# Kernel optimization log

Measured on AMD Instinct MI355X. Metric: run time of the kernel, lower is better.

Reference implementation:

```python
import jax, jax.numpy as jnp
import numpy as np

N_NODES = 50000
N_EDGES = 800000
F = 53
B = 128
H = 4


def _p(key, shape, scale=0.1):
    return jax.random.normal(key, shape, dtype=jnp.float32) * scale


def setup_inputs() -> dict:
    key = jax.random.key(0)
    ks = jax.random.split(key, 40)
    inp = {
        'x': jax.random.normal(ks[0], (N_NODES, F), dtype=jnp.float32),
        'edge_index': jax.random.randint(ks[1], (2, N_EDGES), 0, N_NODES),
        'batch': jnp.sort(jax.random.randint(ks[2], (N_NODES,), 0, B)),
        # GATConv(53 -> 53, heads=4)
        'gat_w': _p(ks[3], (F, H * F)),
        'gat_att_src': _p(ks[4], (H, F)),
        'gat_att_dst': _p(ks[5], (H, F)),
        'gat_bias': _p(ks[6], (H * F,)),
        # GINConv MLP: 53 -> 106 -> 106
        'gin_w1': _p(ks[7], (F, 2 * F)), 'gin_b1': _p(ks[8], (2 * F,)),
        'gin_w2': _p(ks[9], (2 * F, 2 * F)), 'gin_b2': _p(ks[10], (2 * F,)),
        # EdgeConv MLP: 106 -> 106 -> 106
        'ec_w1': _p(ks[11], (2 * F, 2 * F)), 'ec_b1': _p(ks[12], (2 * F,)),
        'ec_w2': _p(ks[13], (2 * F, 2 * F)), 'ec_b2': _p(ks[14], (2 * F,)),
        # per-branch heads
        'fg1_w': _p(ks[15], (4 * F, 256)), 'fg1_b': _p(ks[16], (256,)),
        'fg2_w': _p(ks[17], (256, 128)), 'fg2_b': _p(ks[18], (128,)),
        'fg3_w': _p(ks[19], (2 * F, 256)), 'fg3_b': _p(ks[20], (256,)),
        'fg4_w': _p(ks[21], (256, 128)), 'fg4_b': _p(ks[22], (128,)),
        'fg5_w': _p(ks[23], (2 * F, 256)), 'fg5_b': _p(ks[24], (256,)),
        'fg6_w': _p(ks[25], (256, 128)), 'fg6_b': _p(ks[26], (128,)),
        # final MLP
        'fc1_w': _p(ks[27], (384, 128)), 'fc1_b': _p(ks[28], (128,)),
        'fc2_w': _p(ks[29], (128, 64)), 'fc2_b': _p(ks[30], (64,)),
        'out_w': _p(ks[31], (64, 1)), 'out_b': _p(ks[32], (1,)),
    }
    return inp


def _gat(x, src, dst, w, a_src, a_dst, bias):
    # PyG GATConv with add_self_loops=True, negative_slope=0.2, concat heads
    n = x.shape[0]
    loop = jnp.arange(n)
    s = jnp.concatenate([src, loop])
    d = jnp.concatenate([dst, loop])
    xh = (x @ w).reshape(n, H, F)                      # [N,H,F]
    al_s = jnp.einsum('nhf,hf->nh', xh, a_src)         # [N,H]
    al_d = jnp.einsum('nhf,hf->nh', xh, a_dst)
    e = jax.nn.leaky_relu(al_s[s] + al_d[d], 0.2)      # [E2,H]
    m = jax.ops.segment_max(e, d, num_segments=n)
    ex = jnp.exp(e - m[d])
    z = jax.ops.segment_sum(ex, d, num_segments=n)
    alpha = ex / (z[d] + 1e-16)                        # softmax over in-edges
    msg = xh[s] * alpha[:, :, None]                    # [E2,H,F]
    out = jax.ops.segment_sum(msg, d, num_segments=n)
    return out.reshape(n, H * F) + bias


def _gin(x, src, dst, w1, b1, w2, b2):
    # PyG GINConv, eps=0: nn(x + sum_j x_j)
    n = x.shape[0]
    agg = jax.ops.segment_sum(x[src], dst, num_segments=n)
    h = x + agg
    return jax.nn.relu(h @ w1 + b1) @ w2 + b2


def _edgeconv(x, src, dst, w1, b1, w2, b2):
    # PyG EdgeConv: max_j nn([x_i, x_j - x_i]) at target i
    n = x.shape[0]
    xi = x[dst]
    feat = jnp.concatenate([xi, x[src] - xi], axis=-1)  # [E,2F]
    h = jax.nn.relu(feat @ w1 + b1) @ w2 + b2
    out = jax.ops.segment_max(h, dst, num_segments=n)
    return jnp.where(jnp.isfinite(out), out, 0.0)       # empty segments -> 0


def _gep(x, batch):
    # global mean pool per graph
    s = jax.ops.segment_sum(x, batch, num_segments=B)
    cnt = jax.ops.segment_sum(jnp.ones((x.shape[0],), x.dtype), batch, num_segments=B)
    return s / jnp.maximum(cnt, 1.0)[:, None]


def reference(x, edge_index, batch,
              gat_w, gat_att_src, gat_att_dst, gat_bias,
              gin_w1, gin_b1, gin_w2, gin_b2,
              ec_w1, ec_b1, ec_w2, ec_b2,
              fg1_w, fg1_b, fg2_w, fg2_b, fg3_w, fg3_b,
              fg4_w, fg4_b, fg5_w, fg5_b, fg6_w, fg6_b,
              fc1_w, fc1_b, fc2_w, fc2_b, out_w, out_b):
    relu = jax.nn.relu
    src, dst = edge_index[0], edge_index[1]

    xt = relu(_gat(x, src, dst, gat_w, gat_att_src, gat_att_dst, gat_bias))
    xt = _gep(xt, batch)
    xt = relu(xt @ fg1_w + fg1_b)
    xt = relu(xt @ fg2_w + fg2_b)

    xt2 = relu(_gin(x, src, dst, gin_w1, gin_b1, gin_w2, gin_b2))
    xt2 = _gep(xt2, batch)
    xt2 = relu(xt2 @ fg3_w + fg3_b)
    xt2 = relu(xt2 @ fg4_w + fg4_b)

    xt3 = relu(_edgeconv(x, src, dst, ec_w1, ec_b1, ec_w2, ec_b2))
    xt3 = _gep(xt3, batch)
    xt3 = relu(xt3 @ fg5_w + fg5_b)
    xt3 = relu(xt3 @ fg6_w + fg6_b)

    h = jnp.concatenate([xt, xt2, xt3], axis=1)         # [B,384]
    h = relu(h @ fc1_w + fc1_b)
    h = relu(h @ fc2_w + fc2_b)
    return jax.nn.sigmoid(h @ out_w + out_b)            # [B,1]
```

## Files before the change

kernel.cpp:

```cpp
#include <hip/hip_runtime.h>
#include <hip/hip_bf16.h>
#include <math.h>

#define N_NODES 50000
#define N_EDGES 800000
#define FDIM 53
#define BATCH 128
#define HF 212
#define F2 106
#define POOLW 424
#define NPK2 220
#define PSTR 32
#define ECS 128
#define A4P 256

typedef __attribute__((ext_vector_type(8))) short short8;
typedef __attribute__((ext_vector_type(4))) float f32x4;

__device__ __forceinline__ float leaky02(float x){ return x >= 0.f ? x : 0.2f * x; }

__device__ __forceinline__ short f2bf(float x) {
  unsigned u = __float_as_uint(x);
  unsigned r = (u + 0x7fffu + ((u >> 16) & 1u)) >> 16;
  return (short)r;
}
__device__ __forceinline__ float bf2f(short b) {
  return __uint_as_float(((unsigned)(unsigned short)b) << 16);
}
__device__ __forceinline__ unsigned pk2(float a, float b) {
  union { __hip_bfloat162 h; unsigned u; } c;
  c.h = __float22bfloat162_rn(make_float2(a, b));
  return c.u;
}
__device__ __forceinline__ void ldsbar() {
  __builtin_amdgcn_s_waitcnt(0xC07F);
  __builtin_amdgcn_s_barrier();
}

__global__ void k_prep(const float* __restrict__ ec_w1, const float* __restrict__ ec_b1,
                       const float* __restrict__ gat_w, const float* __restrict__ asrc,
                       const float* __restrict__ adst,
                       float* __restrict__ Wp, float* __restrict__ bp) {
  int idx = blockIdx.x * blockDim.x + threadIdx.x;
  if (idx < FDIM * NPK2) {
    int k = idx / NPK2, j = idx % NPK2;
    float v;
    if (j < F2)            v = ec_w1[k * F2 + j] - ec_w1[(FDIM + k) * F2 + j];
    else if (j < 2 * F2)   v = ec_w1[(FDIM + k) * F2 + (j - F2)];
    else {
      int r = j - 2 * F2;
      int sd = r >> 2, h = r & 3;
      const float* av = sd ? adst : asrc;
      float acc = 0.f;
      for (int f = 0; f < FDIM; ++f)
        acc += gat_w[k * HF + h * FDIM + f] * av[h * FDIM + f];
      v = acc;
    }
    Wp[idx] = v;
  }
  if (idx < NPK2) {
    bp[idx] = (idx < F2) ? ec_b1[idx] : 0.f;
  }
}

#define GM 64
#define GN 110
#define GNP 112
#define APAD 57
__global__ __launch_bounds__(256) void k_gemm(
    const float* __restrict__ x, const float* __restrict__ Wp, const float* __restrict__ bp,
    short* __restrict__ xb, short* __restrict__ Ub, short* __restrict__ Vb,
    float* __restrict__ alS, float* __restrict__ alD) {
  __shared__ float As[GM * APAD];
  __shared__ float Ws[FDIM * GNP];
  int mb = blockIdx.x >> 1, nc = blockIdx.x & 1;
  int m0 = mb * GM, n0 = nc * GN;
  int t = threadIdx.x;
  for (int idx = t; idx < GM * FDIM; idx += 256) {
    int m = idx / FDIM, k = idx % FDIM;
    int gm = m0 + m;
    float v = (gm < N_NODES) ? x[(size_t)gm * FDIM + k] : 0.f;
    As[m * APAD + k] = v;
    if (nc == 0 && gm < N_NODES) xb[(size_t)gm * 64 + k] = f2bf(v);
  }
  for (int idx = t; idx < FDIM * GNP; idx += 256) {
    int k = idx / GNP, n = idx % GNP;
    Ws[idx] = (n < GN) ? Wp[k * NPK2 + n0 + n] : 0.f;
  }
  __syncthreads();
  int tx = t & 15, ty = t >> 4;
  int ms = tx * 4, ns = ty * 7;
  float acc[4][7];
#pragma unroll
  for (int i = 0; i < 4; i++)
#pragma unroll
    for (int j = 0; j < 7; j++) acc[i][j] = 0.f;
  for (int k = 0; k < FDIM; k++) {
    float a0 = As[(ms + 0) * APAD + k];
    float a1 = As[(ms + 1) * APAD + k];
    float a2 = As[(ms + 2) * APAD + k];
    float a3 = As[(ms + 3) * APAD + k];
    float b[7];
#pragma unroll
    for (int j = 0; j < 7; j++) b[j] = Ws[k * GNP + ns + j];
#pragma unroll
    for (int j = 0; j < 7; j++) {
      acc[0][j] += a0 * b[j];
      acc[1][j] += a1 * b[j];
      acc[2][j] += a2 * b[j];
      acc[3][j] += a3 * b[j];
    }
  }
  float bj[7];
#pragma unroll
  for (int j = 0; j < 7; j++) {
    int g = n0 + ns + j;
    bj[j] = (g < NPK2) ? bp[g] : 0.f;
  }
#pragma unroll
  for (int i = 0; i < 4; i++) {
    int gm = m0 + ms + i;
    if (gm >= N_NODES) break;
#pragma unroll
    for (int j = 0; j < 7; j++) {
      int g = n0 + ns + j;
      float v = acc[i][j] + bj[j];
      if (g < F2)             Ub[(size_t)gm * ECS + g] = f2bf(v);
      else if (g < 2 * F2)    Vb[(size_t)gm * ECS + (g - F2)] = f2bf(v);
      else if (g < 2 * F2 + 4) alS[gm * 4 + (g - 2 * F2)] = v;
      else if (g < NPK2)      alD[gm * 4 + (g - 2 * F2 - 4)] = v;
    }
  }
}

#define SCAN_BLOCKS ((N_NODES + 255) / 256)

__global__ void k_hist(const int* __restrict__ ei, int* __restrict__ histP) {
  int t = blockIdx.x * blockDim.x + threadIdx.x;
  if (t < N_EDGES) atomicAdd(&histP[ei[N_EDGES + t] << 5], 1);
}

__global__ __launch_bounds__(256) void k_scan1(const int* __restrict__ histP,
                                               const int* __restrict__ batch,
                                               int* __restrict__ rp, int* __restrict__ bsum,
                                               int* __restrict__ start) {
  __shared__ int buf[256];
  int tid = threadIdx.x;
  int idx = blockIdx.x * 256 + tid;
  int v = (idx < N_NODES) ? histP[idx << 5] : 0;
  buf[tid] = v;
  __syncthreads();
  for (int off = 1; off < 256; off <<= 1) {
    int t2 = (tid >= off) ? buf[tid - off] : 0;
    __syncthreads();
    buf[tid] += t2;
    __syncthreads();
  }
  if (idx < N_NODES) rp[idx] = buf[tid] - v;
  if (tid == 255) bsum[blockIdx.x] = buf[255];
  if (idx < N_NODES) {
    int b = batch[idx];
    if (idx == 0)
      for (int g = 0; g <= b; g++) start[g] = 0;
    int bn = (idx + 1 < N_NODES) ? batch[idx + 1] : BATCH;
    for (int g = b + 1; g <= bn; g++) start[g] = idx + 1;
  }
}

__global__ __launch_bounds__(256) void k_scan3(const int* __restrict__ bsum,
                                               int* __restrict__ rp, int* __restrict__ histP) {
  __shared__ int buf[256];
  int tid = threadIdx.x;
  int v = (tid < SCAN_BLOCKS) ? bsum[tid] : 0;
  buf[tid] = v;
  __syncthreads();
  for (int off = 1; off < 256; off <<= 1) {
    int t2 = (tid >= off) ? buf[tid - off] : 0;
    __syncthreads();
    buf[tid] += t2;
    __syncthreads();
  }
  int boff = (blockIdx.x == 0) ? 0 : buf[blockIdx.x - 1];
  int idx = blockIdx.x * 256 + tid;
  if (idx < N_NODES) {
    int o = rp[idx] + boff;
    rp[idx] = o;
    histP[idx << 5] = o;
  }
  if (idx == 0) rp[N_NODES] = N_EDGES;
}

__global__ void k_scatter(const int* __restrict__ ei, int* __restrict__ histP,
                          int* __restrict__ colidx) {
  int e = blockIdx.x * blockDim.x + threadIdx.x;
  if (e >= N_EDGES) return;
  int d = ei[N_EDGES + e];
  int pos = atomicAdd(&histP[d << 5], 1);
  colidx[pos] = ei[e];
}

#define GCH 20
__global__ __launch_bounds__(256) void k_gatgin(
    const short* __restrict__ xb, const float* __restrict__ alS, const float* __restrict__ alD,
    const int* __restrict__ rp, const int* __restrict__ colidx,
    short* __restrict__ agg4, float* __restrict__ agg) {
  int wid = threadIdx.x >> 6, lane = threadIdx.x & 63;
  bool fa = lane < FDIM;
  int i0 = blockIdx.x * GCH;
  int iend = min(i0 + GCH, N_NODES);
  __shared__ int rpG[GCH + 1];
  __shared__ int sL[4][64];
  __shared__ float4 eL[4][64];
  {
    int t = threadIdx.x, nn = iend - i0;
    if (t <= nn) rpG[t] = rp[i0 + t];
  }
  __syncthreads();
  for (int i = i0 + wid; i < iend; i += 4) {
    int base = rpG[i - i0], deg = rpG[i - i0 + 1] - base;
    float4 adv = *(const float4*)(alD + (size_t)i * 4);
    float4 asv = *(const float4*)(alS + (size_t)i * 4);
    float aldi[4] = {adv.x, adv.y, adv.z, adv.w};
    float exs[4];
    exs[0] = __expf(leaky02(asv.x + aldi[0]));
    exs[1] = __expf(leaky02(asv.y + aldi[1]));
    exs[2] = __expf(leaky02(asv.z + aldi[2]));
    exs[3] = __expf(leaky02(asv.w + aldi[3]));
    float xiv = fa ? bf2f(xb[(size_t)i * 64 + lane]) : 0.f;
    float ag0 = exs[0] * xiv, ag1 = exs[1] * xiv, ag2 = exs[2] * xiv, ag3 = exs[3] * xiv;
    float ax = xiv;
    float zl[4] = {0.f, 0.f, 0.f, 0.f};

    for (int c0 = 0; c0 < deg; c0 += 64) {
      int cn = min(64, deg - c0);
      int s = 0;
      float ex0 = 0.f, ex1 = 0.f, ex2 = 0.f, ex3 = 0.f;
      if (lane < cn) {
        s = colidx[base + c0 + lane];
        float4 av = *(const float4*)(alS + (size_t)s * 4);
        ex0 = __expf(leaky02(av.x + aldi[0]));
        ex1 = __expf(leaky02(av.y + aldi[1]));
        ex2 = __expf(leaky02(av.z + aldi[2]));
        ex3 = __expf(leaky02(av.w + aldi[3]));
        zl[0] += ex0; zl[1] += ex1; zl[2] += ex2; zl[3] += ex3;
      }
      sL[wid][lane] = s;
      eL[wid][lane] = make_float4(ex0, ex1, ex2, ex3);
      for (int jj = 0; jj < cn; jj += 4) {
        int4 s4 = *(const int4*)&sL[wid][jj];
        int sj[4] = {s4.x, s4.y, s4.z, s4.w};
        float4 e0 = eL[wid][jj + 0];
        float4 e1 = eL[wid][jj + 1];
        float4 e2 = eL[wid][jj + 2];
        float4 e3 = eL[wid][jj + 3];
        float xg[4];
#pragma unroll
        for (int q = 0; q < 4; q++)
          xg[q] = fa ? bf2f(xb[(size_t)sj[q] * 64 + lane]) : 0.f;
        ag0 += e0.x * xg[0] + e1.x * xg[1] + e2.x * xg[2] + e3.x * xg[3];
        ag1 += e0.y * xg[0] + e1.y * xg[1] + e2.y * xg[2] + e3.y * xg[3];
        ag2 += e0.z * xg[0] + e1.z * xg[1] + e2.z * xg[2] + e3.z * xg[3];
        ag3 += e0.w * xg[0] + e1.w * xg[1] + e2.w * xg[2] + e3.w * xg[3];
#pragma unroll
        for (int q = 0; q < 4; q++)
          if (jj + q < cn) ax += xg[q];
      }
    }
#pragma unroll
    for (int off = 32; off >= 1; off >>= 1)
#pragma unroll
      for (int h = 0; h < 4; h++) zl[h] += __shfl_xor(zl[h], off);
    {
      float z0 = zl[0] + exs[0] + 1e-16f;
      float z1 = zl[1] + exs[1] + 1e-16f;
      float z2 = zl[2] + exs[2] + 1e-16f;
      float z3 = zl[3] + exs[3] + 1e-16f;
      short* ar = agg4 + (size_t)i * A4P;
      ar[0 * 64 + lane] = fa ? f2bf(ag0 / z0) : (short)0;
      ar[1 * 64 + lane] = fa ? f2bf(ag1 / z1) : (short)0;
      ar[2 * 64 + lane] = fa ? f2bf(ag2 / z2) : (short)0;
      ar[3 * 64 + lane] = fa ? f2bf(ag3 / z3) : (short)0;
      if (fa) agg[(size_t)i * FDIM + lane] = ax;
    }
  }
}

#define BTS 72
__global__ __launch_bounds__(256) void k_gt(
    const short* __restrict__ agg4, const float* __restrict__ gat_w,
    const float* __restrict__ gat_b, const int* __restrict__ batch,
    float* __restrict__ pooled) {
  __shared__ short Bt[4 * 56 * BTS];
  __shared__ float psum[4 * 224];
  __shared__ int batL[64];
  int m0 = blockIdx.x * 64;
  int t = threadIdx.x;
  for (int idx = t; idx < 4 * 224; idx += 256) psum[idx] = 0.f;
  if (t < 64) batL[t] = batch[min(m0 + t, N_NODES - 1)];
  for (int idx = t; idx < 4 * 64 * 56; idx += 256) {
    int n = idx % 56, kk = (idx / 56) & 63, h = idx / (56 * 64);
    short v = (kk < FDIM && n < FDIM) ? f2bf(gat_w[kk * HF + h * FDIM + n]) : (short)0;
    Bt[(h * 56 + n) * BTS + kk] = v;
  }
  __syncthreads();
  const int lane = t & 63, wid = t >> 6;
  const int n16 = lane & 15, quad = lane >> 4;
  const int mrow0 = wid * 16;
  const int bmin = batL[0];
  const bool uni = (batL[0] == batL[63]);
  const size_t abase = (size_t)(m0 + mrow0 + n16) * A4P;
#pragma unroll
  for (int h = 0; h < 4; h++) {
    short8 af0 = *(const short8*)(agg4 + abase + h * 64 + quad * 8);
    short8 af1 = *(const short8*)(agg4 + abase + h * 64 + 32 + quad * 8);
#pragma unroll
    for (int nt = 0; nt < 4; nt++) {
      short8 b0 = *(const short8*)&Bt[(h * 56 + nt * 16 + n16) * BTS + quad * 8];
      short8 b1 = *(const short8*)&Bt[(h * 56 + nt * 16 + n16) * BTS + 32 + quad * 8];
      f32x4 acc = {0.f, 0.f, 0.f, 0.f};
      acc = __builtin_amdgcn_mfma_f32_16x16x32_bf16(af0, b0, acc, 0, 0, 0);
      acc = __builtin_amdgcn_mfma_f32_16x16x32_bf16(af1, b1, acc, 0, 0, 0);
      int jn = nt * 16 + n16;
      bool jv = jn < FDIM;
      float bj = jv ? gat_b[h * FDIM + jn] : 0.f;
      if (uni) {
        float s = 0.f;
#pragma unroll
        for (int r = 0; r < 4; r++) {
          int gm = m0 + mrow0 + quad * 4 + r;
          if (gm < N_NODES) s += fmaxf(acc[r] + bj, 0.f);
        }
        s += __shfl_xor(s, 16);
        s += __shfl_xor(s, 32);
        if (quad == 0 && jv && s != 0.f) atomicAdd(&psum[h * 56 + jn], s);
      } else {
        float pj = 0.f; int curb = -1;
#pragma unroll
        for (int r = 0; r < 4; r++) {
          int lm = mrow0 + quad * 4 + r;
          int gm = m0 + lm;
          if (gm < N_NODES) {
            float o = fmaxf(acc[r] + bj, 0.f);
            int b = batL[lm];
            if (b != curb) {
              if (curb >= 0 && jv) {
                int slot = curb - bmin;
                if (slot >= 0 && slot < 4) atomicAdd(&psum[slot * 224 + h * 56 + jn], pj);
                else atomicAdd(&pooled[(size_t)curb * POOLW + h * FDIM + jn], pj);
              }
              curb = b; pj = o;
            } else {
              pj += o;
            }
          }
        }
        if (curb >= 0 && jv) {
          int slot = curb - bmin;
          if (slot >= 0 && slot < 4) atomicAdd(&psum[slot * 224 + h * 56 + jn], pj);
          else atomicAdd(&pooled[(size_t)curb * POOLW + h * FDIM + jn], pj);
        }
      }
    }
  }
  __syncthreads();
  for (int idx = t; idx < 4 * 224; idx += 256) {
    int slot = idx / 224, c = idx % 224;
    int h = c / 56, jn = c % 56;
    float v = psum[idx];
    int b = bmin + slot;
    if (jn < FDIM && b < BATCH && v != 0.f)
      atomicAdd(&pooled[(size_t)b * POOLW + h * FDIM + jn], v);
  }
}

#define A2PAD 111
__global__ __launch_bounds__(256) void k_gin(
    const float* __restrict__ agg,
    const float* __restrict__ w1, const float* __restrict__ b1,
    const float* __restrict__ w2, const float* __restrict__ b2,
    const int* __restrict__ batch, float* __restrict__ pooled) {
  __shared__ float B1[F2 * 112];
  __shared__ float Hs[64 * A2PAD];
  __shared__ float psum[4 * 112];
  float* As = B1;
  float* Ws1 = B1 + 64 * APAD;
  int m0 = blockIdx.x * 64;
  int t = threadIdx.x;
  for (int idx = t; idx < 4 * 112; idx += 256) psum[idx] = 0.f;
  for (int idx = t; idx < 64 * FDIM; idx += 256) {
    int m = idx / FDIM, k = idx % FDIM;
    int gm = m0 + m;
    As[m * APAD + k] = (gm < N_NODES) ? agg[(size_t)gm * FDIM + k] : 0.f;
  }
  for (int idx = t; idx < FDIM * 112; idx += 256) {
    int k = idx / 112, n = idx % 112;
    Ws1[idx] = (n < F2) ? w1[k * F2 + n] : 0.f;
  }
  __syncthreads();
  int tx = t & 15, ty = t >> 4;
  int ms = tx * 4, ns = ty * 7;
  {
    float acc[4][7];
#pragma unroll
    for (int i = 0; i < 4; i++)
#pragma unroll
      for (int j = 0; j < 7; j++) acc[i][j] = 0.f;
    for (int k = 0; k < FDIM; k++) {
      float a0 = As[(ms + 0) * APAD + k];
      float a1 = As[(ms + 1) * APAD + k];
      float a2 = As[(ms + 2) * APAD + k];
      float a3 = As[(ms + 3) * APAD + k];
      float b[7];
#pragma unroll
      for (int j = 0; j < 7; j++) b[j] = Ws1[k * 112 + ns + j];
#pragma unroll
      for (int j = 0; j < 7; j++) {
        acc[0][j] += a0 * b[j];
        acc[1][j] += a1 * b[j];
        acc[2][j] += a2 * b[j];
        acc[3][j] += a3 * b[j];
      }
    }
#pragma unroll
    for (int i = 0; i < 4; i++) {
#pragma unroll
      for (int j = 0; j < 7; j++) {
        int n = ns + j;
        if (n < F2) Hs[(ms + i) * A2PAD + n] = fmaxf(acc[i][j] + b1[n], 0.f);
      }
    }
  }
  __syncthreads();
  for (int idx = t; idx < F2 * 112; idx += 256) {
    int k = idx / 112, n = idx % 112;
    B1[idx] = (n < F2) ? w2[k * F2 + n] : 0.f;
  }
  __syncthreads();
  float acc[4][7];
#pragma unroll
  for (int i = 0; i < 4; i++)
#pragma unroll
    for (int j = 0; j < 7; j++) acc[i][j] = 0.f;
  for (int k = 0; k < F2; k++) {
    float a0 = Hs[(ms + 0) * A2PAD + k];
    float a1 = Hs[(ms + 1) * A2PAD + k];
    float a2 = Hs[(ms + 2) * A2PAD + k];
    float a3 = Hs[(ms + 3) * A2PAD + k];
    float b[7];
#pragma unroll
    for (int j = 0; j < 7; j++) b[j] = B1[k * 112 + ns + j];
#pragma unroll
    for (int j = 0; j < 7; j++) {
      acc[0][j] += a0 * b[j];
      acc[1][j] += a1 * b[j];
      acc[2][j] += a2 * b[j];
      acc[3][j] += a3 * b[j];
    }
  }
  float b2n[7];
#pragma unroll
  for (int j = 0; j < 7; j++) {
    int n = ns + j;
    b2n[j] = (n < F2) ? b2[n] : 0.f;
  }
  int bmin = batch[m0];
  float pj[7];
#pragma unroll
  for (int j = 0; j < 7; j++) pj[j] = 0.f;
  int curb = -1;
#pragma unroll
  for (int i = 0; i < 4; i++) {
    int gm = m0 + ms + i;
    if (gm >= N_NODES) break;
    int b = batch[gm];
    if (b != curb) {
      if (curb >= 0) {
        int slot = curb - bmin;
        if (slot >= 0 && slot < 4) {
#pragma unroll
          for (int j = 0; j < 7; j++)
            if (ns + j < F2) atomicAdd(&psum[slot * 112 + ns + j], pj[j]);
        } else {
          float* pg = pooled + (size_t)curb * POOLW + HF;
#pragma unroll
          for (int j = 0; j < 7; j++)
            if (ns + j < F2) atomicAdd(&pg[ns + j], pj[j]);
        }
      }
      curb = b;
#pragma unroll
      for (int j = 0; j < 7; j++)
        pj[j] = (ns + j < F2) ? fmaxf(acc[i][j] + b2n[j], 0.f) : 0.f;
    } else {
#pragma unroll
      for (int j = 0; j < 7; j++)
        if (ns + j < F2) pj[j] += fmaxf(acc[i][j] + b2n[j], 0.f);
    }
  }
  if (curb >= 0) {
    int slot = curb - bmin;
    if (slot >= 0 && slot < 4) {
#pragma unroll
      for (int j = 0; j < 7; j++)
        if (ns + j < F2) atomicAdd(&psum[slot * 112 + ns + j], pj[j]);
    } else {
      float* pg = pooled + (size_t)curb * POOLW + HF;
#pragma unroll
      for (int j = 0; j < 7; j++)
        if (ns + j < F2) atomicAdd(&pg[ns + j], pj[j]);
    }
  }
  __syncthreads();
  for (int idx = t; idx < 4 * 112; idx += 256) {
    int slot = idx / 112, n = idx % 112;
    float v = psum[idx];
    int b = bmin + slot;
    if (n < F2 && b < BATCH && v != 0.f)
      atomicAdd(&pooled[(size_t)b * POOLW + HF + n], v);
  }
}

#define ECH 25
__global__ __launch_bounds__(256) void k_ec(
    const short* __restrict__ Ub, const short* __restrict__ Vb,
    const float* __restrict__ w2, const float* __restrict__ b2,
    const int* __restrict__ rp, const int* __restrict__ colidx,
    const int* __restrict__ batch, float* __restrict__ pooled) {
  const int t = threadIdx.x;
  const int lane = t & 63, wid = t >> 6;
  const int n16 = lane & 15, quad = lane >> 4;
  const int nt = (wid == 3) ? 1 : 2;

  const int i0 = blockIdx.x * ECH;
  const int iend = min(i0 + ECH, N_NODES);
  const int nn = iend - i0;

  __shared__ int rpL[ECH + 1];
  __shared__ int batL[ECH];

  short8 Bh[2][4];
  for (int tt = 0; tt < 2; tt++) {
    int ucol = (wid * 2 + tt) * 16 + n16;
    for (int kc = 0; kc < 4; kc++) {
      short8 vh;
#pragma unroll
      for (int jv = 0; jv < 8; jv++) {
        int kk = kc * 32 + quad * 8 + jv;
        float w = (ucol < F2 && kk < F2) ? w2[kk * F2 + ucol] : 0.f;
        vh[jv] = f2bf(w);
      }
      Bh[tt][kc] = vh;
    }
  }
  float b2v[2];
#pragma unroll
  for (int tt = 0; tt < 2; tt++) {
    int u = (wid * 2 + tt) * 16 + n16;
    b2v[tt] = (u < F2) ? b2[u] : 0.f;
  }

  if (t <= nn) rpL[t] = rp[i0 + t];
  if (t < nn) batL[t] = batch[i0 + t];
  __syncthreads();

  __shared__ short hs[2][16 * 16 * 8];
  union SU { short8 s; unsigned u[4]; };
  const int es = t & 15, kg = t >> 4;
  const int k0 = kg * 8;

  float sm0 = 0.f, sm1 = 0.f;
  int curb = -1;
  const int u0 = (wid * 2) * 16 + n16;
  const int u1 = (wid * 2 + 1) * 16 + n16;

  auto advance = [&](int& ii, int& ttb, int& bb, int& dd) -> bool {
    ttb++;
    if (ttb * 16 < dd) return true;
    ttb = 0;
    for (ii = ii + 1; ii < iend; ii++) {
      bb = rpL[ii - i0]; dd = rpL[ii - i0 + 1] - bb;
      if (dd > 0) return true;
    }
    return false;
  };

  int i = i0, tb = 0, base = 0, deg = 0;
  bool have = false;
  for (; i < iend; i++) {
    base = rpL[i - i0]; deg = rpL[i - i0 + 1] - base;
    if (deg > 0) { have = true; break; }
  }
  short8 pu8{}, pv8{};
  int i1 = i, tb1 = 0, base1 = base, deg1 = deg;
  bool have1 = false;
  int sc = 0;
  if (have) {
    pu8 = *(const short8*)(Ub + (size_t)i * ECS + k0);
    int s0 = colidx[base + ((es < deg) ? es : 0)];
    pv8 = *(const short8*)(Vb + (size_t)s0 * ECS + k0);
    have1 = advance(i1, tb1, base1, deg1);
    if (have1) {
      int eg = tb1 * 16 + es;
      sc = colidx[base1 + ((eg < deg1) ? eg : 0)];
    }
  }

  float Uc[8];
  float vmax0 = -1e30f, vmax1 = -1e30f;
  int parity = 0;
  while (have) {
    if (tb == 0) {
#pragma unroll
      for (int j = 0; j < 8; j++) Uc[j] = bf2f(pu8[j]);
    }
    SU w;
#pragma unroll
    for (int p = 0; p < 4; p++) {
      bool kv = (k0 + 2 * p) < F2;
      float h0 = kv ? fmaxf(Uc[2 * p]     + bf2f(pv8[2 * p]),     0.f) : 0.f;
      float h1 = kv ? fmaxf(Uc[2 * p + 1] + bf2f(pv8[2 * p + 1]), 0.f) : 0.f;
      w.u[p] = pk2(h0, h1);
    }
    *(short8*)&hs[parity][(kg * 16 + es) * 8] = w.s;

    int i2 = i1, tb2 = tb1, base2 = base1, deg2 = deg1;
    bool have2 = false;
    int scN = 0;
    if (have1) {
      if (tb1 == 0) pu8 = *(const short8*)(Ub + (size_t)i1 * ECS + k0);
      pv8 = *(const short8*)(Vb + (size_t)sc * ECS + k0);
      have2 = advance(i2, tb2, base2, deg2);
      if (have2) {
        int eg2 = tb2 * 16 + es;
        scN = colidx[base2 + ((eg2 < deg2) ? eg2 : 0)];
      }
    }

    ldsbar();
    f32x4 a0 = {0.f, 0.f, 0.f, 0.f}, a1 = {0.f, 0.f, 0.f, 0.f};
#pragma unroll
    for (int kc = 0; kc < 4; kc++) {
      short8 af = *(const short8*)&hs[parity][((kc * 4 + quad) * 16 + n16) * 8];
      a0 = __builtin_amdgcn_mfma_f32_16x16x32_bf16(af, Bh[0][kc], a0, 0, 0, 0);
      if (nt > 1)
        a1 = __builtin_amdgcn_mfma_f32_16x16x32_bf16(af, Bh[1][kc], a1, 0, 0, 0);
    }
#pragma unroll
    for (int r = 0; r < 4; r++) {
      int er = tb * 16 + quad * 4 + r;
      if (er < deg) { vmax0 = fmaxf(vmax0, a0[r]); vmax1 = fmaxf(vmax1, a1[r]); }
    }
    if (!have1 || i1 != i) {
      vmax0 = fmaxf(vmax0, __shfl_xor(vmax0, 16));
      vmax0 = fmaxf(vmax0, __shfl_xor(vmax0, 32));
      vmax1 = fmaxf(vmax1, __shfl_xor(vmax1, 16));
      vmax1 = fmaxf(vmax1, __shfl_xor(vmax1, 32));
      float o0 = fmaxf(vmax0 + b2v[0], 0.f);
      float o1 = fmaxf(vmax1 + b2v[1], 0.f);
      int b = batL[i - i0];
      if (b != curb) {
        if (curb >= 0 && quad == 0) {
          float* pg = pooled + (size_t)curb * POOLW + HF + F2;
          if (u0 < F2) atomicAdd(&pg[u0], sm0);
          if (nt > 1 && u1 < F2) atomicAdd(&pg[u1], sm1);
        }
        curb = b; sm0 = o0; sm1 = o1;
      } else {
        sm0 += o0; sm1 += o1;
      }
      vmax0 = -1e30f; vmax1 = -1e30f;
    }
    i = i1; tb = tb1; base = base1; deg = deg1; have = have1;
    i1 = i2; tb1 = tb2; base1 = base2; deg1 = deg2; have1 = have2;
    sc = scN;
    parity ^= 1;
  }
  if (curb >= 0 && quad == 0) {
    float* pg = pooled + (size_t)curb * POOLW + HF + F2;
    if (u0 < F2) atomicAdd(&pg[u0], sm0);
    if (nt > 1 && u1 < F2) atomicAdd(&pg[u1], sm1);
  }
}

__global__ __launch_bounds__(256) void k_heads(
    const float* __restrict__ pooled, const int* __restrict__ start,
    const float* __restrict__ fg1_w, const float* __restrict__ fg1_b,
    const float* __restrict__ fg2_w, const float* __restrict__ fg2_b,
    const float* __restrict__ fg3_w, const float* __restrict__ fg3_b,
    const float* __restrict__ fg4_w, const float* __restrict__ fg4_b,
    const float* __restrict__ fg5_w, const float* __restrict__ fg5_b,
    const float* __restrict__ fg6_w, const float* __restrict__ fg6_b,
    const float* __restrict__ fc1_w, const float* __restrict__ fc1_b,
    const float* __restrict__ fc2_w, const float* __restrict__ fc2_b,
    const float* __restrict__ out_w, const float* __restrict__ out_b,
    float* __restrict__ out) {
  int g = blockIdx.x, t = threadIdx.x;
  __shared__ float in[POOLW];
  __shared__ float mid[256];
  __shared__ float cat[384];
  __shared__ float h1[128];
  __shared__ float h2[64];
  float c = fmaxf((float)(start[g + 1] - start[g]), 1.f);
  for (int idx = t; idx < POOLW; idx += 256)
    in[idx] = pooled[(size_t)g * POOLW + idx] / c;
  __syncthreads();
  const float* w1s[3] = {fg1_w, fg3_w, fg5_w};
  const float* b1s[3] = {fg1_b, fg3_b, fg5_b};
  const float* w2s[3] = {fg2_w, fg4_w, fg6_w};
  const float* b2s[3] = {fg2_b, fg4_b, fg6_b};
  const int off[4] = {0, HF, HF + F2, POOLW};
  for (int br = 0; br < 3; br++) {
    int kin = off[br + 1] - off[br];
    const float* iv = &in[off[br]];
    float a = b1s[br][t];
    const float* W = w1s[br];
    for (int k = 0; k < kin; k++) a += iv[k] * W[k * 256 + t];
    mid[t] = fmaxf(a, 0.f);
    __syncthreads();
    if (t < 128) {
      float b = b2s[br][t];
      const float* W2 = w2s[br];
      for (int k = 0; k < 256; k++) b += mid[k] * W2[k * 128 + t];
      cat[br * 128 + t] = fmaxf(b, 0.f);
    }
    __syncthreads();
  }
  if (t < 128) {
    float a = fc1_b[t];
    for (int k = 0; k < 384; k++) a += cat[k] * fc1_w[k * 128 + t];
    h1[t] = fmaxf(a, 0.f);
  }
  __syncthreads();
  if (t < 64) {
    float a = fc2_b[t];
    for (int k = 0; k < 128; k++) a += h1[k] * fc2_w[k * 64 + t];
    h2[t] = fmaxf(a, 0.f);
  }
  __syncthreads();
  if (t == 0) {
    float a = out_b[0];
    for (int k = 0; k < 64; k++) a += h2[k] * out_w[k];
    out[g] = 1.f / (1.f + __expf(-a));
  }
}

extern "C" void kernel_launch(void* const* d_in, const int* in_sizes, int n_in,
                              void* d_out, int out_size, void* d_ws, size_t ws_size,
                              hipStream_t stream) {
  const float* x      = (const float*)d_in[0];
  const int*   ei     = (const int*)d_in[1];
  const int*   batch  = (const int*)d_in[2];
  const float* gat_w  = (const float*)d_in[3];
  const float* asrc   = (const float*)d_in[4];
  const float* adst   = (const float*)d_in[5];
  const float* gat_b  = (const float*)d_in[6];
  const float* gin_w1 = (const float*)d_in[7];
  const float* gin_b1 = (const float*)d_in[8];
  const float* gin_w2 = (const float*)d_in[9];
  const float* gin_b2 = (const float*)d_in[10];
  const float* ec_w1  = (const float*)d_in[11];
  const float* ec_b1  = (const float*)d_in[12];
  const float* ec_w2  = (const float*)d_in[13];
  const float* ec_b2  = (const float*)d_in[14];
  const float* fg1_w = (const float*)d_in[15]; const float* fg1_b = (const float*)d_in[16];
  const float* fg2_w = (const float*)d_in[17]; const float* fg2_b = (const float*)d_in[18];
  const float* fg3_w = (const float*)d_in[19]; const float* fg3_b = (const float*)d_in[20];
  const float* fg4_w = (const float*)d_in[21]; const float* fg4_b = (const float*)d_in[22];
  const float* fg5_w = (const float*)d_in[23]; const float* fg5_b = (const float*)d_in[24];
  const float* fg6_w = (const float*)d_in[25]; const float* fg6_b = (const float*)d_in[26];
  const float* fc1_w = (const float*)d_in[27]; const float* fc1_b = (const float*)d_in[28];
  const float* fc2_w = (const float*)d_in[29]; const float* fc2_b = (const float*)d_in[30];
  const float* out_w = (const float*)d_in[31]; const float* out_b = (const float*)d_in[32];
  float* out = (float*)d_out;

  char* ws = (char*)d_ws;
  size_t off = 0;
  auto alloc = [&](size_t bytes) -> void* {
    void* p = ws + off;
    off = (off + bytes + 255) & ~(size_t)255;
    return p;
  };
  size_t zoff0 = off;
  int*   histP  = (int*)alloc((size_t)N_NODES * PSTR * sizeof(int));
  float* pooled = (float*)alloc((size_t)BATCH * POOLW * sizeof(float));
  size_t zbytes = off - zoff0;
  int*   rp     = (int*)alloc((N_NODES + 1) * sizeof(int));
  int*   start  = (int*)alloc((BATCH + 1) * sizeof(int));
  int*   bsum   = (int*)alloc(256 * sizeof(int));
  int*   colidx = (int*)alloc(N_EDGES * sizeof(int));
  short* xb     = (short*)alloc((size_t)N_NODES * 64 * sizeof(short));
  float* alS    = (float*)alloc((size_t)N_NODES * 4 * sizeof(float));
  float* alD    = (float*)alloc((size_t)N_NODES * 4 * sizeof(float));
  short* Ubuf   = (short*)alloc((size_t)N_NODES * ECS * sizeof(short));
  short* Vbuf   = (short*)alloc((size_t)N_NODES * ECS * sizeof(short));
  short* agg4   = (short*)alloc((size_t)(N_NODES + 64) * A4P * sizeof(short));
  float* agg    = (float*)alloc((size_t)N_NODES * FDIM * sizeof(float));
  float* Wp     = (float*)alloc((size_t)FDIM * NPK2 * sizeof(float));
  float* bpk    = (float*)alloc(NPK2 * sizeof(float));
  (void)ws_size; (void)in_sizes; (void)n_in; (void)out_size;

  hipMemsetAsync(ws + zoff0, 0, zbytes, stream);

  k_prep<<<(FDIM * NPK2 + 255) / 256, 256, 0, stream>>>(ec_w1, ec_b1, gat_w, asrc, adst,
                                                        Wp, bpk);
  k_gemm<<<((N_NODES + GM - 1) / GM) * 2, 256, 0, stream>>>(x, Wp, bpk,
                                                            xb, Ubuf, Vbuf, alS, alD);
  k_hist<<<(N_EDGES + 255) / 256, 256, 0, stream>>>(ei, histP);
  k_scan1<<<SCAN_BLOCKS, 256, 0, stream>>>(histP, batch, rp, bsum, start);
  k_scan3<<<SCAN_BLOCKS, 256, 0, stream>>>(bsum, rp, histP);
  k_scatter<<<(N_EDGES + 255) / 256, 256, 0, stream>>>(ei, histP, colidx);

  k_gatgin<<<(N_NODES + GCH - 1) / GCH, 256, 0, stream>>>(xb, alS, alD, rp, colidx,
                                                          agg4, agg);
  k_ec<<<(N_NODES + ECH - 1) / ECH, 256, 0, stream>>>(Ubuf, Vbuf, ec_w2, ec_b2, rp, colidx, batch, pooled);
  k_gt<<<(N_NODES + 63) / 64, 256, 0, stream>>>(agg4, gat_w, gat_b, batch, pooled);
  k_gin<<<(N_NODES + 63) / 64, 256, 0, stream>>>(agg, gin_w1, gin_b1, gin_w2, gin_b2,
                                                 batch, pooled);

  k_heads<<<BATCH, 256, 0, stream>>>(pooled, start,
                                     fg1_w, fg1_b, fg2_w, fg2_b, fg3_w, fg3_b,
                                     fg4_w, fg4_b, fg5_w, fg5_b, fg6_w, fg6_b,
                                     fc1_w, fc1_b, fc2_w, fc2_b, out_w, out_b, out);
}
```

Measured before the change: 649.0 us.

## Move GIN MLP to bf16 MFMA with hi/lo split-precision activations

The GIN MLP kernel's scalar fp32 GEMMs are replaced with MFMA 16x16x32 bf16 instructions. The aggregated input and the hidden layer are each stored as a bf16 hi/lo pair to keep accuracy near fp32, while the weights are rounded to plain bf16. The gather kernel now writes the padded bf16 hi/lo buffer instead of fp32, and a fast path pools with shuffles when a tile sits in a single graph. This trades some precision in the weights for much cheaper matrix math and lower register pressure.

```diff
diff --git a/kernel.cpp b/kernel.cpp
--- a/kernel.cpp
+++ b/kernel.cpp
@@ -203,7 +203,7 @@
 __global__ __launch_bounds__(256) void k_gatgin(
     const short* __restrict__ xb, const float* __restrict__ alS, const float* __restrict__ alD,
     const int* __restrict__ rp, const int* __restrict__ colidx,
-    short* __restrict__ agg4, float* __restrict__ agg) {
+    short* __restrict__ agg4, short* __restrict__ aggb) {
   int wid = threadIdx.x >> 6, lane = threadIdx.x & 63;
   bool fa = lane < FDIM;
   int i0 = blockIdx.x * GCH;
@@ -280,7 +280,12 @@
       ar[1 * 64 + lane] = fa ? f2bf(ag1 / z1) : (short)0;
       ar[2 * 64 + lane] = fa ? f2bf(ag2 / z2) : (short)0;
       ar[3 * 64 + lane] = fa ? f2bf(ag3 / z3) : (short)0;
-      if (fa) agg[(size_t)i * FDIM + lane] = ax;
+      float axv = fa ? ax : 0.f;
+      short hi = f2bf(axv);
+      float lov = axv - bf2f(hi);
+      short* br = aggb + (size_t)i * 128;
+      br[lane]      = fa ? hi : (short)0;
+      br[64 + lane] = fa ? f2bf(lov) : (short)0;
     }
   }
 }
@@ -373,141 +378,127 @@
   }
 }
 
-#define A2PAD 111
-__global__ __launch_bounds__(256) void k_gin(
-    const float* __restrict__ agg,
+#define H1S 132
+#define BWS 132
+__global__ __launch_bounds__(256) void k_ginm(
+    const short* __restrict__ aggb,
     const float* __restrict__ w1, const float* __restrict__ b1,
     const float* __restrict__ w2, const float* __restrict__ b2,
     const int* __restrict__ batch, float* __restrict__ pooled) {
-  __shared__ float B1[F2 * 112];
-  __shared__ float Hs[64 * A2PAD];
+  __shared__ short h1hi[64 * H1S];
+  __shared__ short h1lo[64 * H1S];
+  __shared__ short Btw[112 * BWS];
   __shared__ float psum[4 * 112];
-  float* As = B1;
-  float* Ws1 = B1 + 64 * APAD;
+  __shared__ int batL[64];
   int m0 = blockIdx.x * 64;
   int t = threadIdx.x;
   for (int idx = t; idx < 4 * 112; idx += 256) psum[idx] = 0.f;
-  for (int idx = t; idx < 64 * FDIM; idx += 256) {
-    int m = idx / FDIM, k = idx % FDIM;
-    int gm = m0 + m;
-    As[m * APAD + k] = (gm < N_NODES) ? agg[(size_t)gm * FDIM + k] : 0.f;
-  }
-  for (int idx = t; idx < FDIM * 112; idx += 256) {
-    int k = idx / 112, n = idx % 112;
-    Ws1[idx] = (n < F2) ? w1[k * F2 + n] : 0.f;
-  }
-  __syncthreads();
-  int tx = t & 15, ty = t >> 4;
-  int ms = tx * 4, ns = ty * 7;
+  if (t < 64) batL[t] = batch[min(m0 + t, N_NODES - 1)];
+  for (int idx = t; idx < 64 * H1S / 2; idx += 256) {
+    ((int*)h1hi)[idx] = 0;
+    ((int*)h1lo)[idx] = 0;
+  }
+  for (int idx = t; idx < 112 * 128; idx += 256) {
+    int n = idx >> 7, kk = idx & 127;
+    int ks = kk & 63;
+    short v = (ks < FDIM && n < F2) ? f2bf(w1[ks * F2 + n]) : (short)0;
+    Btw[n * BWS + kk] = v;
+  }
+  __syncthreads();
+  const int lane = t & 63, wid = t >> 6;
+  const int n16 = lane & 15, quad = lane >> 4;
+  const int mrow0 = wid * 16;
+  const int bmin = batL[0];
+  const bool uni = (batL[0] == batL[63]);
   {
-    float acc[4][7];
-#pragma unroll
-    for (int i = 0; i < 4; i++)
-#pragma unroll
-      for (int j = 0; j < 7; j++) acc[i][j] = 0.f;
-    for (int k = 0; k < FDIM; k++) {
-      float a0 = As[(ms + 0) * APAD + k];
-      float a1 = As[(ms + 1) * APAD + k];
-      float a2 = As[(ms + 2) * APAD + k];
-      float a3 = As[(ms + 3) * APAD + k];
-      float b[7];
-#pragma unroll
-      for (int j = 0; j < 7; j++) b[j] = Ws1[k * 112 + ns + j];
-#pragma unroll
-      for (int j = 0; j < 7; j++) {
-        acc[0][j] += a0 * b[j];
-        acc[1][j] += a1 * b[j];
-        acc[2][j] += a2 * b[j];
-        acc[3][j] += a3 * b[j];
-      }
-    }
-#pragma unroll
-    for (int i = 0; i < 4; i++) {
-#pragma unroll
-      for (int j = 0; j < 7; j++) {
-        int n = ns + j;
-        if (n < F2) Hs[(ms + i) * A2PAD + n] = fmaxf(acc[i][j] + b1[n], 0.f);
-      }
-    }
-  }
-  __syncthreads();
-  for (int idx = t; idx < F2 * 112; idx += 256) {
-    int k = idx / 112, n = idx % 112;
-    B1[idx] = (n < F2) ? w2[k * F2 + n] : 0.f;
-  }
-  __syncthreads();
-  float acc[4][7];
-#pragma unroll
-  for (int i = 0; i < 4; i++)
-#pragma unroll
-    for (int j = 0; j < 7; j++) acc[i][j] = 0.f;
-  for (int k = 0; k < F2; k++) {
-    float a0 = Hs[(ms + 0) * A2PAD + k];
-    float a1 = Hs[(ms + 1) * A2PAD + k];
-    float a2 = Hs[(ms + 2) * A2PAD + k];
-    float a3 = Hs[(ms + 3) * A2PAD + k];
-    float b[7];
-#pragma unroll
-    for (int j = 0; j < 7; j++) b[j] = B1[k * 112 + ns + j];
-#pragma unroll
-    for (int j = 0; j < 7; j++) {
-      acc[0][j] += a0 * b[j];
-      acc[1][j] += a1 * b[j];
-      acc[2][j] += a2 * b[j];
-      acc[3][j] += a3 * b[j];
-    }
-  }
-  float b2n[7];
-#pragma unroll
-  for (int j = 0; j < 7; j++) {
-    int n = ns + j;
-    b2n[j] = (n < F2) ? b2[n] : 0.f;
-  }
-  int bmin = batch[m0];
-  float pj[7];
-#pragma unroll
-  for (int j = 0; j < 7; j++) pj[j] = 0.f;
-  int curb = -1;
-#pragma unroll
-  for (int i = 0; i < 4; i++) {
-    int gm = m0 + ms + i;
-    if (gm >= N_NODES) break;
-    int b = batch[gm];
-    if (b != curb) {
-      if (curb >= 0) {
+    const size_t abase = (size_t)(m0 + mrow0 + n16) * 128;
+    short8 a[4];
+#pragma unroll
+    for (int f = 0; f < 4; f++)
+      a[f] = *(const short8*)(aggb + abase + f * 32 + quad * 8);
+#pragma unroll
+    for (int nt = 0; nt < 7; nt++) {
+      f32x4 acc = {0.f, 0.f, 0.f, 0.f};
+#pragma unroll
+      for (int f = 0; f < 4; f++) {
+        short8 bf = *(const short8*)&Btw[(nt * 16 + n16) * BWS + f * 32 + quad * 8];
+        acc = __builtin_amdgcn_mfma_f32_16x16x32_bf16(a[f], bf, acc, 0, 0, 0);
+      }
+      int jn = nt * 16 + n16;
+      if (jn < F2) {
+        float bj = b1[jn];
+#pragma unroll
+        for (int r = 0; r < 4; r++) {
+          int row = mrow0 + quad * 4 + r;
+          float v = fmaxf(acc[r] + bj, 0.f);
+          short hi = f2bf(v);
+          h1hi[row * H1S + jn] = hi;
+          h1lo[row * H1S + jn] = f2bf(v - bf2f(hi));
+        }
+      }
+    }
+  }
+  __syncthreads();
+  for (int idx = t; idx < 112 * 128; idx += 256) {
+    int n = idx >> 7, kk = idx & 127;
+    short v = (kk < F2 && n < F2) ? f2bf(w2[kk * F2 + n]) : (short)0;
+    Btw[n * BWS + kk] = v;
+  }
+  __syncthreads();
+  short8 ah[4], al[4];
+#pragma unroll
+  for (int f = 0; f < 4; f++) {
+    ah[f] = *(const short8*)&h1hi[(mrow0 + n16) * H1S + f * 32 + quad * 8];
+    al[f] = *(const short8*)&h1lo[(mrow0 + n16) * H1S + f * 32 + quad * 8];
+  }
+#pragma unroll
+  for (int nt = 0; nt < 7; nt++) {
+    f32x4 acc = {0.f, 0.f, 0.f, 0.f};
+#pragma unroll
+    for (int f = 0; f < 4; f++) {
+      short8 bf = *(const short8*)&Btw[(nt * 16 + n16) * BWS + f * 32 + quad * 8];
+      acc = __builtin_amdgcn_mfma_f32_16x16x32_bf16(ah[f], bf, acc, 0, 0, 0);
+      acc = __builtin_amdgcn_mfma_f32_16x16x32_bf16(al[f], bf, acc, 0, 0, 0);
+    }
+    int jn = nt * 16 + n16;
+    bool jv = jn < F2;
+    float bj = jv ? b2[jn] : 0.f;
+    if (uni) {
+      float s = 0.f;
+#pragma unroll
+      for (int r = 0; r < 4; r++) {
+        int gm = m0 + mrow0 + quad * 4 + r;
+        if (gm < N_NODES) s += fmaxf(acc[r] + bj, 0.f);
+      }
+      s += __shfl_xor(s, 16);
+      s += __shfl_xor(s, 32);
+      if (quad == 0 && jv && s != 0.f) atomicAdd(&psum[jn], s);
+    } else {
+      float pj = 0.f; int curb = -1;
+#pragma unroll
+      for (int r = 0; r < 4; r++) {
+        int lm = mrow0 + quad * 4 + r;
+        int gm = m0 + lm;
+        if (gm < N_NODES) {
+          float o = fmaxf(acc[r] + bj, 0.f);
+          int b = batL[lm];
+          if (b != curb) {
+            if (curb >= 0 && jv) {
+              int slot = curb - bmin;
+              if (slot >= 0 && slot < 4) atomicAdd(&psum[slot * 112 + jn], pj);
+              else atomicAdd(&pooled[(size_t)curb * POOLW + HF + jn], pj);
+            }
+            curb = b; pj = o;
+          } else {
+            pj += o;
+          }
+        }
+      }
+      if (curb >= 0 && jv) {
         int slot = curb - bmin;
-        if (slot >= 0 && slot < 4) {
-#pragma unroll
-          for (int j = 0; j < 7; j++)
-            if (ns + j < F2) atomicAdd(&psum[slot * 112 + ns + j], pj[j]);
-        } else {
-          float* pg = pooled + (size_t)curb * POOLW + HF;
-#pragma unroll
-          for (int j = 0; j < 7; j++)
-            if (ns + j < F2) atomicAdd(&pg[ns + j], pj[j]);
-        }
-      }
-      curb = b;
-#pragma unroll
-      for (int j = 0; j < 7; j++)
-        pj[j] = (ns + j < F2) ? fmaxf(acc[i][j] + b2n[j], 0.f) : 0.f;
-    } else {
-#pragma unroll
-      for (int j = 0; j < 7; j++)
-        if (ns + j < F2) pj[j] += fmaxf(acc[i][j] + b2n[j], 0.f);
-    }
-  }
-  if (curb >= 0) {
-    int slot = curb - bmin;
-    if (slot >= 0 && slot < 4) {
-#pragma unroll
-      for (int j = 0; j < 7; j++)
-        if (ns + j < F2) atomicAdd(&psum[slot * 112 + ns + j], pj[j]);
-    } else {
-      float* pg = pooled + (size_t)curb * POOLW + HF;
-#pragma unroll
-      for (int j = 0; j < 7; j++)
-        if (ns + j < F2) atomicAdd(&pg[ns + j], pj[j]);
+        if (slot >= 0 && slot < 4) atomicAdd(&psum[slot * 112 + jn], pj);
+        else atomicAdd(&pooled[(size_t)curb * POOLW + HF + jn], pj);
+      }
     }
   }
   __syncthreads();
@@ -794,7 +785,7 @@
   short* Ubuf   = (short*)alloc((size_t)N_NODES * ECS * sizeof(short));
   short* Vbuf   = (short*)alloc((size_t)N_NODES * ECS * sizeof(short));
   short* agg4   = (short*)alloc((size_t)(N_NODES + 64) * A4P * sizeof(short));
-  float* agg    = (float*)alloc((size_t)N_NODES * FDIM * sizeof(float));
+  short* aggb   = (short*)alloc((size_t)(N_NODES + 64) * 128 * sizeof(short));
   float* Wp     = (float*)alloc((size_t)FDIM * NPK2 * sizeof(float));
   float* bpk    = (float*)alloc(NPK2 * sizeof(float));
   (void)ws_size; (void)in_sizes; (void)n_in; (void)out_size;
@@ -811,11 +802,11 @@
   k_scatter<<<(N_EDGES + 255) / 256, 256, 0, stream>>>(ei, histP, colidx);
 
   k_gatgin<<<(N_NODES + GCH - 1) / GCH, 256, 0, stream>>>(xb, alS, alD, rp, colidx,
-                                                          agg4, agg);
+                                                          agg4, aggb);
   k_ec<<<(N_NODES + ECH - 1) / ECH, 256, 0, stream>>>(Ubuf, Vbuf, ec_w2, ec_b2, rp, colidx, batch, pooled);
   k_gt<<<(N_NODES + 63) / 64, 256, 0, stream>>>(agg4, gat_w, gat_b, batch, pooled);
-  k_gin<<<(N_NODES + 63) / 64, 256, 0, stream>>>(agg, gin_w1, gin_b1, gin_w2, gin_b2,
-                                                 batch, pooled);
+  k_ginm<<<(N_NODES + 63) / 64, 256, 0, stream>>>(aggb, gin_w1, gin_b1, gin_w2, gin_b2,
+                                                  batch, pooled);
 
   k_heads<<<BATCH, 256, 0, stream>>>(pooled, start,
                                      fg1_w, fg1_b, fg2_w, fg2_b, fg3_w, fg3_b,
```

Result: faster. 634.7 us (-2.2%).
